# Optimization experiments

Measured on AMD Instinct MI355X. Metric: run time of the kernel, lower is better.

Reference implementation:

```python
import jax, jax.numpy as jnp
import numpy as np

N_COMPONENTS = 16
N_FEATURES = 64
N_SAMPLES = 200000


def setup_inputs() -> dict:
    key = jax.random.key(0)
    k_data, k_means, k_cov = jax.random.split(key, 3)
    data = jax.random.normal(k_data, (N_SAMPLES, N_FEATURES), dtype=jnp.float32)
    weights = jnp.ones((N_COMPONENTS,), dtype=jnp.float32) / N_COMPONENTS
    means = jax.random.normal(k_means, (N_COMPONENTS, N_FEATURES), dtype=jnp.float32)
    # SPD covariances: A A^T / d + I (module inits to identity; use realistic SPD here)
    A = jax.random.normal(k_cov, (N_COMPONENTS, N_FEATURES, N_FEATURES), dtype=jnp.float32)
    covariances = jnp.einsum('kij,klj->kil', A, A) / N_FEATURES + jnp.eye(N_FEATURES, dtype=jnp.float32)
    return {"data": data, "weights": weights, "means": means, "covariances": covariances}


def reference(data, weights, means, covariances):
    # data: [N, d]; weights: [K]; means: [K, d]; covariances: [K, d, d]
    d = data.shape[1]
    L = jnp.linalg.cholesky(covariances)                      # [K, d, d]
    diff = data[None, :, :] - means[:, None, :]               # [K, N, d]
    # Solve L y = diff^T per component (batched triangular solve)
    y = jax.scipy.linalg.solve_triangular(L, jnp.swapaxes(diff, -1, -2), lower=True)  # [K, d, N]
    maha = jnp.sum(y * y, axis=1)                             # [K, N]
    half_logdet = jnp.sum(jnp.log(jnp.diagonal(L, axis1=-2, axis2=-1)), axis=-1)      # [K]
    log2pi = jnp.log(jnp.array(2.0 * np.pi, dtype=data.dtype))
    log_probs = -0.5 * (maha + d * log2pi) - half_logdet[:, None]                     # [K, N]
    weighted_log_probs = log_probs + jnp.log(weights)[:, None]
    log_sum_exp = jax.scipy.special.logsumexp(weighted_log_probs, axis=0)             # [N]
    return jnp.sum(log_sum_exp)
```

## Files before the change

### kernel.cpp

```cpp
#include <hip/hip_runtime.h>
#include <hip/hip_bf16.h>
#include <math.h>

#define NF 64
#define NC 16
#define MAIN_BLOCKS 256
#define MAIN_WAVES  13
#define TPW 4

typedef __bf16 bf16x8 __attribute__((ext_vector_type(8)));
typedef float f32x4 __attribute__((ext_vector_type(4)));
typedef unsigned int u32;

__device__ __forceinline__ void stage16(const void* gsrc, void* ldst) {
    __builtin_amdgcn_global_load_lds(
        (const __attribute__((address_space(1))) u32*)gsrc,
        (__attribute__((address_space(3))) u32*)ldst,
        16, 0, 0);
}

__global__ __launch_bounds__(256) void gmm_precompute(
    const float* __restrict__ cov,
    const float* __restrict__ means,
    const float* __restrict__ weights,
    __hip_bfloat16* __restrict__ g,
    float* __restrict__ t,
    float* __restrict__ Cc)
{
    const int w = threadIdx.x >> 6;
    const int c = threadIdx.x & 63;
    const int k = blockIdx.x;

    __shared__ __align__(16) float LT[NF][68];
    __shared__ float Xs[NF][65];
    __shared__ __align__(16) float wb2[2][68];
    __shared__ __align__(16) float gw2[2][68];

    float a_loc[16];
    {
        const float* src = cov + (long)k * NF * NF + (w * 16) * NF + c;
        #pragma unroll
        for (int r = 0; r < 16; ++r)
            a_loc[r] = src[r * NF];
    }

    float s_loc[16];
    #pragma unroll
    for (int r = 0; r < 16; ++r)
        s_loc[r] = (w * 16 + r == c) ? 1.0f : 0.0f;

    float logdiag  = 0.0f;
    float rsq_prev = 0.0f;

    #pragma unroll 1
    for (int q = 0; q < 4; ++q) {
        #pragma unroll
        for (int jj = 0; jj < 16; ++jj) {
            const int j = q * 16 + jj;
            float* wb = wb2[jj & 1];
            float* gw = gw2[jj & 1];

            if (w == q) wb[c] = a_loc[jj];
            if (j > 0) {
                const int pw = (jj == 0) ? (q - 1) : q;
                const int pi = (jj == 0) ? 15 : (jj - 1);
                if (w == pw) {
                    float gv = s_loc[pi] * rsq_prev;
                    gw[c] = gv;
                    Xs[j - 1][c] = gv;
                }
            }
            __syncthreads();

            float ajc = wb[c];
            float d   = wb[j];
            float sq  = sqrtf(d);
            float rsq = __builtin_amdgcn_rcpf(sq);
            float rd  = __builtin_amdgcn_rcpf(d);
            logdiag += 0.5f * __logf(d);
            rsq_prev = rsq;
            LT[j][c] = ajc * rsq;
            float beta = ajc * rd;
            const float4* wv = (const float4*)(wb + w * 16);
            #pragma unroll
            for (int rr = 0; rr < 16; rr += 4) {
                float4 v = wv[rr >> 2];
                a_loc[rr]     = fmaf(-v.x, beta, a_loc[rr]);
                a_loc[rr + 1] = fmaf(-v.y, beta, a_loc[rr + 1]);
                a_loc[rr + 2] = fmaf(-v.z, beta, a_loc[rr + 2]);
                a_loc[rr + 3] = fmaf(-v.w, beta, a_loc[rr + 3]);
            }

            if (j > 0) {
                float gc = gw[c];
                const float4* lv4 = (const float4*)(&LT[j - 1][w * 16]);
                #pragma unroll
                for (int rr = 0; rr < 16; rr += 4) {
                    float4 v = lv4[rr >> 2];
                    s_loc[rr]     = fmaf(-v.x, gc, s_loc[rr]);
                    s_loc[rr + 1] = fmaf(-v.y, gc, s_loc[rr + 1]);
                    s_loc[rr + 2] = fmaf(-v.z, gc, s_loc[rr + 2]);
                    s_loc[rr + 3] = fmaf(-v.w, gc, s_loc[rr + 3]);
                }
            }
        }
    }

    if (w == 3) Xs[63][c] = s_loc[15] * rsq_prev;
    __syncthreads();

    {
        __hip_bfloat16* grow = g + ((long)(k * NF + c)) * NF;
        #pragma unroll
        for (int h = 0; h < 2; ++h) {
            int jb = w * 2 + h;
            bf16x8 v;
            #pragma unroll
            for (int u = 0; u < 8; ++u)
                v[u] = (__bf16)Xs[c][jb * 8 + u];
            *(bf16x8*)(grow + ((jb ^ (c & 7)) * 8)) = v;
        }
    }

    if (w == 0) {
        const float* mu = means + k * NF;
        float a0 = 0.0f, a1 = 0.0f;
        #pragma unroll
        for (int j = 0; j < NF; j += 2) {
            a0 = fmaf(Xs[c][j],     mu[j],     a0);
            a1 = fmaf(Xs[c][j + 1], mu[j + 1], a1);
        }
        t[k * NF + c] = a0 + a1;
        if (c == 0)
            Cc[k] = __logf(weights[k]) - 0.5f * (float)NF * 1.8378770664093453f - logdiag;
    }
}

__global__ __launch_bounds__(832) void gmm_main(
    const float* __restrict__ data,
    const char* __restrict__ gsw,
    const float* __restrict__ t,
    const float* __restrict__ Cc,
    float* __restrict__ partials,
    int nTiles, int N, int totalWaves)
{
    __shared__ __align__(16) char gbuf[NC * 8192];
    __shared__ __align__(16) float nt_lds[NC * NF];
    __shared__ float cc_lds[NC];

    const int tidx = threadIdx.x;
    const int w    = tidx >> 6;
    const int lane = tidx & 63;
    const int l15  = lane & 15;
    const int lg   = lane >> 4;

    for (int i = w; i < NC; i += MAIN_WAVES) {
        const char* src = gsw + (size_t)i * 8192;
        char* dst = gbuf + (size_t)i * 8192;
        #pragma unroll
        for (int u = 0; u < 8; ++u)
            stage16(src + u * 1024 + lane * 16, dst + u * 1024);
    }

    for (int i = tidx; i < NC * NF; i += 64 * MAIN_WAVES) nt_lds[i] = -t[i];
    if (tidx < NC) cc_lds[tidx] = Cc[tidx];

    const int gid = blockIdx.x * MAIN_WAVES + w;

    int offA[4], offB[4];
    #pragma unroll
    for (int rc = 0; rc < 4; ++rc) {
        int row = rc * 16 + l15;
        offA[rc] = row * 128 + ((lg       ^ (l15 & 7)) * 16);
        offB[rc] = row * 128 + (((lg + 4) ^ (l15 & 7)) * 16);
    }

    bf16x8 xf[TPW][2];
    if (gid < nTiles) {
        const long base = (long)gid * (TPW * 16);
        #pragma unroll
        for (int st = 0; st < TPW; ++st) {
            long row = base + st * 16 + l15;
            if (row > (long)N - 1) row = (long)N - 1;
            const float* xp = data + row * NF + lg * 8;
            float4 a0 = *(const float4*)(xp);
            float4 a1 = *(const float4*)(xp + 4);
            float4 b0 = *(const float4*)(xp + 32);
            float4 b1 = *(const float4*)(xp + 36);
            bf16x8 f0, f1;
            f0[0] = (__bf16)a0.x; f0[1] = (__bf16)a0.y;
            f0[2] = (__bf16)a0.z; f0[3] = (__bf16)a0.w;
            f0[4] = (__bf16)a1.x; f0[5] = (__bf16)a1.y;
            f0[6] = (__bf16)a1.z; f0[7] = (__bf16)a1.w;
            f1[0] = (__bf16)b0.x; f1[1] = (__bf16)b0.y;
            f1[2] = (__bf16)b0.z; f1[3] = (__bf16)b0.w;
            f1[4] = (__bf16)b1.x; f1[5] = (__bf16)b1.y;
            f1[6] = (__bf16)b1.z; f1[7] = (__bf16)b1.w;
            xf[st][0] = f0;
            xf[st][1] = f1;
        }
    }

    __syncthreads();

    float wavePartial = 0.0f;

    #pragma unroll 1
    for (int tile = gid; tile < nTiles; tile += totalWaves) {
        const long base = (long)tile * (TPW * 16);
        if (tile != gid) {
            #pragma unroll
            for (int st = 0; st < TPW; ++st) {
                long row = base + st * 16 + l15;
                if (row > (long)N - 1) row = (long)N - 1;
                const float* xp = data + row * NF + lg * 8;
                float4 a0 = *(const float4*)(xp);
                float4 a1 = *(const float4*)(xp + 4);
                float4 b0 = *(const float4*)(xp + 32);
                float4 b1 = *(const float4*)(xp + 36);
                bf16x8 f0, f1;
                f0[0] = (__bf16)a0.x; f0[1] = (__bf16)a0.y;
                f0[2] = (__bf16)a0.z; f0[3] = (__bf16)a0.w;
                f0[4] = (__bf16)a1.x; f0[5] = (__bf16)a1.y;
                f0[6] = (__bf16)a1.z; f0[7] = (__bf16)a1.w;
                f1[0] = (__bf16)b0.x; f1[1] = (__bf16)b0.y;
                f1[2] = (__bf16)b0.z; f1[3] = (__bf16)b0.w;
                f1[4] = (__bf16)b1.x; f1[5] = (__bf16)b1.y;
                f1[6] = (__bf16)b1.z; f1[7] = (__bf16)b1.w;
                xf[st][0] = f0;
                xf[st][1] = f1;
            }
        }

        float m[TPW], s[TPW];
        #pragma unroll
        for (int st = 0; st < TPW; ++st) { m[st] = -INFINITY; s[st] = 0.0f; }

        #pragma unroll 2
        for (int ii = 0; ii < NC; ++ii) {
            const int kk = (ii + w) & (NC - 1);
            float mah[TPW];
            #pragma unroll
            for (int st = 0; st < TPW; ++st) mah[st] = 0.0f;

            const char* gk = gbuf + kk * 8192;
            const float* ntk = &nt_lds[kk * NF];

            #pragma unroll
            for (int rc = 0; rc < 2; ++rc) {
                bf16x8 ga = *(const bf16x8*)(gk + offA[rc]);
                f32x4 ntv = *(const f32x4*)(ntk + rc * 16 + lg * 4);
                #pragma unroll
                for (int st = 0; st < TPW; ++st) {
                    f32x4 acc = ntv;
                    acc = __builtin_amdgcn_mfma_f32_16x16x32_bf16(ga, xf[st][0], acc, 0, 0, 0);
                    mah[st] = fmaf(acc[0], acc[0], mah[st]);
                    mah[st] = fmaf(acc[1], acc[1], mah[st]);
                    mah[st] = fmaf(acc[2], acc[2], mah[st]);
                    mah[st] = fmaf(acc[3], acc[3], mah[st]);
                }
            }
            #pragma unroll
            for (int rc = 2; rc < 4; ++rc) {
                bf16x8 ga = *(const bf16x8*)(gk + offA[rc]);
                bf16x8 gb = *(const bf16x8*)(gk + offB[rc]);
                f32x4 ntv = *(const f32x4*)(ntk + rc * 16 + lg * 4);
                #pragma unroll
                for (int st = 0; st < TPW; ++st) {
                    f32x4 acc = ntv;
                    acc = __builtin_amdgcn_mfma_f32_16x16x32_bf16(ga, xf[st][0], acc, 0, 0, 0);
                    acc = __builtin_amdgcn_mfma_f32_16x16x32_bf16(gb, xf[st][1], acc, 0, 0, 0);
                    mah[st] = fmaf(acc[0], acc[0], mah[st]);
                    mah[st] = fmaf(acc[1], acc[1], mah[st]);
                    mah[st] = fmaf(acc[2], acc[2], mah[st]);
                    mah[st] = fmaf(acc[3], acc[3], mah[st]);
                }
            }

            float Ck = cc_lds[kk];
            float wlp[TPW];
            float dmax = -INFINITY;
            #pragma unroll
            for (int st = 0; st < TPW; ++st) {
                float v = mah[st];
                v += __shfl_xor(v, 16);
                v += __shfl_xor(v, 32);
                wlp[st] = fmaf(-0.5f, v, Ck);
                dmax = fmaxf(dmax, wlp[st] - m[st]);
            }
            if (__any(dmax > 60.0f)) {
                #pragma unroll
                for (int st = 0; st < TPW; ++st) {
                    float mn = fmaxf(m[st], wlp[st]);
                    s[st] = s[st] * __expf(m[st] - mn) + __expf(wlp[st] - mn);
                    m[st] = mn;
                }
            } else {
                #pragma unroll
                for (int st = 0; st < TPW; ++st)
                    s[st] += __expf(wlp[st] - m[st]);
            }
        }

        if (lg == 0) {
            #pragma unroll
            for (int st = 0; st < TPW; ++st) {
                long sid = base + st * 16 + l15;
                if (sid < (long)N)
                    wavePartial += m[st] + __logf(s[st]);
            }
        }
    }

    #pragma unroll
    for (int off = 1; off < 64; off <<= 1)
        wavePartial += __shfl_xor(wavePartial, off);
    if (lane == 0)
        partials[gid] = wavePartial;
}

__global__ __launch_bounds__(256) void gmm_reduce(
    const float* __restrict__ partials, int n, float* __restrict__ out)
{
    float s = 0.0f;
    for (int i = threadIdx.x; i < n; i += 256)
        s += partials[i];
    #pragma unroll
    for (int off = 1; off < 64; off <<= 1)
        s += __shfl_xor(s, off);
    __shared__ float sm[4];
    const int wave = threadIdx.x >> 6;
    const int lane = threadIdx.x & 63;
    if (lane == 0) sm[wave] = s;
    __syncthreads();
    if (threadIdx.x == 0)
        out[0] = (sm[0] + sm[1]) + (sm[2] + sm[3]);
}

extern "C" void kernel_launch(void* const* d_in, const int* in_sizes, int n_in,
                              void* d_out, int out_size, void* d_ws, size_t ws_size,
                              hipStream_t stream)
{
    const float* data    = (const float*)d_in[0];
    const float* weights = (const float*)d_in[1];
    const float* means   = (const float*)d_in[2];
    const float* cov     = (const float*)d_in[3];

    const int N = in_sizes[0] / NF;

    char* ws = (char*)d_ws;
    __hip_bfloat16* g = (__hip_bfloat16*)ws;
    float* t          = (float*)(ws + 131072);
    float* Cc         = (float*)(ws + 131072 + 4096);
    float* partials   = (float*)(ws + 131072 + 4096 + 64);

    const int nTiles     = (N + TPW * 16 - 1) / (TPW * 16);
    const int totalWaves = MAIN_BLOCKS * MAIN_WAVES;

    gmm_precompute<<<NC, 256, 0, stream>>>(cov, means, weights, g, t, Cc);
    gmm_main<<<MAIN_BLOCKS, 64 * MAIN_WAVES, 0, stream>>>(
        data, (const char*)g, t, Cc, partials, nTiles, N, totalWaves);
    gmm_reduce<<<1, 256, 0, stream>>>(partials, totalWaves, (float*)d_out);
}
```

Measured before the change: 63.77 us.

## Block the Cholesky/inverse precompute two columns per barrier step

The per-component Cholesky factorization and triangular inverse in the precompute kernel now process two columns per iteration, using a 2x2 blocked update. This halves the number of __syncthreads barriers in the serial 64-step loop. The cost is extra shared buffers and more arithmetic per step. The precompute is a small serial part of the total, and reordering the floating-point operations may slightly change rounding.

Result: faster. 62.24 us (-2.4%).

```diff
diff --git a/kernel.cpp b/kernel.cpp
--- a/kernel.cpp
+++ b/kernel.cpp
@@ -33,8 +33,10 @@
 
     __shared__ __align__(16) float LT[NF][68];
     __shared__ float Xs[NF][65];
-    __shared__ __align__(16) float wb2[2][68];
-    __shared__ __align__(16) float gw2[2][68];
+    __shared__ __align__(16) float wbA2[2][68];
+    __shared__ __align__(16) float wbB2[2][68];
+    __shared__ __align__(16) float gwA2[2][68];
+    __shared__ __align__(16) float gwB2[2][68];
 
     float a_loc[16];
     {
@@ -49,64 +51,92 @@
     for (int r = 0; r < 16; ++r)
         s_loc[r] = (w * 16 + r == c) ? 1.0f : 0.0f;
 
-    float logdiag  = 0.0f;
-    float rsq_prev = 0.0f;
+    float logdiag = 0.0f;
+    float gvA = 0.0f, gvB = 0.0f;
 
     #pragma unroll 1
     for (int q = 0; q < 4; ++q) {
         #pragma unroll
-        for (int jj = 0; jj < 16; ++jj) {
-            const int j = q * 16 + jj;
-            float* wb = wb2[jj & 1];
-            float* gw = gw2[jj & 1];
-
-            if (w == q) wb[c] = a_loc[jj];
+        for (int h = 0; h < 8; ++h) {
+            const int j = q * 16 + 2 * h;
+            float* wbA = wbA2[h & 1];
+            float* wbB = wbB2[h & 1];
+            float* gwA = gwA2[h & 1];
+            float* gwB = gwB2[h & 1];
+
+            if (w == q) {
+                wbA[c] = a_loc[2 * h];
+                wbB[c] = a_loc[2 * h + 1];
+            }
             if (j > 0) {
-                const int pw = (jj == 0) ? (q - 1) : q;
-                const int pi = (jj == 0) ? 15 : (jj - 1);
+                const int pw = (h == 0) ? (q - 1) : q;
                 if (w == pw) {
-                    float gv = s_loc[pi] * rsq_prev;
-                    gw[c] = gv;
-                    Xs[j - 1][c] = gv;
+                    gwA[c] = gvA;  Xs[j - 2][c] = gvA;
+                    gwB[c] = gvB;  Xs[j - 1][c] = gvB;
                 }
             }
             __syncthreads();
 
-            float ajc = wb[c];
-            float d   = wb[j];
-            float sq  = sqrtf(d);
-            float rsq = __builtin_amdgcn_rcpf(sq);
-            float rd  = __builtin_amdgcn_rcpf(d);
-            logdiag += 0.5f * __logf(d);
-            rsq_prev = rsq;
-            LT[j][c] = ajc * rsq;
-            float beta = ajc * rd;
-            const float4* wv = (const float4*)(wb + w * 16);
-            #pragma unroll
-            for (int rr = 0; rr < 16; rr += 4) {
-                float4 v = wv[rr >> 2];
-                a_loc[rr]     = fmaf(-v.x, beta, a_loc[rr]);
-                a_loc[rr + 1] = fmaf(-v.y, beta, a_loc[rr + 1]);
-                a_loc[rr + 2] = fmaf(-v.z, beta, a_loc[rr + 2]);
-                a_loc[rr + 3] = fmaf(-v.w, beta, a_loc[rr + 3]);
+            float ajc = wbA[c];
+            float bjc = wbB[c];
+            float d0  = wbA[j];
+            float a1j = wbA[j + 1];
+            float b1j = wbB[j + 1];
+            float rd0 = __builtin_amdgcn_rcpf(d0);
+            float k0  = a1j * rd0;
+            float d1  = fmaf(-a1j, k0, b1j);
+            float rd1 = __builtin_amdgcn_rcpf(d1);
+            float rsq0 = __builtin_amdgcn_rcpf(sqrtf(d0));
+            float rsq1 = __builtin_amdgcn_rcpf(sqrtf(d1));
+            logdiag += 0.5f * (__logf(d0) + __logf(d1));
+            float w1c = fmaf(-ajc, k0, bjc);
+            LT[j][c]     = ajc * rsq0;
+            LT[j + 1][c] = w1c * rsq1;
+            float beta0 = ajc * rd0;
+            float beta1 = w1c * rd1;
+            {
+                const float4* wvA = (const float4*)(wbA + w * 16);
+                const float4* wvB = (const float4*)(wbB + w * 16);
+                #pragma unroll
+                for (int rr = 0; rr < 16; rr += 4) {
+                    float4 vA = wvA[rr >> 2];
+                    float4 vB = wvB[rr >> 2];
+                    float t0 = fmaf(-vA.x, k0, vB.x);
+                    float t1 = fmaf(-vA.y, k0, vB.y);
+                    float t2 = fmaf(-vA.z, k0, vB.z);
+                    float t3 = fmaf(-vA.w, k0, vB.w);
+                    a_loc[rr]     = fmaf(-t0, beta1, fmaf(-vA.x, beta0, a_loc[rr]));
+                    a_loc[rr + 1] = fmaf(-t1, beta1, fmaf(-vA.y, beta0, a_loc[rr + 1]));
+                    a_loc[rr + 2] = fmaf(-t2, beta1, fmaf(-vA.z, beta0, a_loc[rr + 2]));
+                    a_loc[rr + 3] = fmaf(-t3, beta1, fmaf(-vA.w, beta0, a_loc[rr + 3]));
+                }
             }
 
             if (j > 0) {
-                float gc = gw[c];
-                const float4* lv4 = (const float4*)(&LT[j - 1][w * 16]);
+                float gA = gwA[c];
+                float gB = gwB[c];
+                const float4* lvA = (const float4*)(&LT[j - 2][w * 16]);
+                const float4* lvB = (const float4*)(&LT[j - 1][w * 16]);
                 #pragma unroll
                 for (int rr = 0; rr < 16; rr += 4) {
-                    float4 v = lv4[rr >> 2];
-                    s_loc[rr]     = fmaf(-v.x, gc, s_loc[rr]);
-                    s_loc[rr + 1] = fmaf(-v.y, gc, s_loc[rr + 1]);
-                    s_loc[rr + 2] = fmaf(-v.z, gc, s_loc[rr + 2]);
-                    s_loc[rr + 3] = fmaf(-v.w, gc, s_loc[rr + 3]);
-                }
-            }
-        }
-    }
-
-    if (w == 3) Xs[63][c] = s_loc[15] * rsq_prev;
+                    float4 vA = lvA[rr >> 2];
+                    float4 vB = lvB[rr >> 2];
+                    s_loc[rr]     = fmaf(-vB.x, gB, fmaf(-vA.x, gA, s_loc[rr]));
+                    s_loc[rr + 1] = fmaf(-vB.y, gB, fmaf(-vA.y, gA, s_loc[rr + 1]));
+                    s_loc[rr + 2] = fmaf(-vB.z, gB, fmaf(-vA.z, gA, s_loc[rr + 2]));
+                    s_loc[rr + 3] = fmaf(-vB.w, gB, fmaf(-vA.w, gA, s_loc[rr + 3]));
+                }
+            }
+
+            if (w == q) {
+                float l10 = a1j * rsq0;
+                gvA = s_loc[2 * h] * rsq0;
+                gvB = fmaf(-l10, gvA, s_loc[2 * h + 1]) * rsq1;
+            }
+        }
+    }
+
+    if (w == 3) { Xs[62][c] = gvA; Xs[63][c] = gvB; }
     __syncthreads();
 
     {
```
